# Performance work log

Measured on AMD Instinct MI355X. Metric: run time of the kernel, lower is better.

The kernel has to match this reference:

```python
import jax, jax.numpy as jnp
import numpy as np

N_NODES = 40000
N_EDGES = 640000
IN_DIM = 128
HID_DIM = 128


def _glorot(key, shape):
    fan_in, fan_out = shape[1], shape[0]
    lim = np.sqrt(6.0 / (fan_in + fan_out))
    return jax.random.uniform(key, shape, jnp.float32, -lim, lim)


def setup_inputs() -> dict:
    key = jax.random.key(0)
    ks = jax.random.split(key, 8)
    x = jax.random.normal(ks[0], (N_NODES, IN_DIM), dtype=jnp.float32)
    edge_index = jax.random.randint(ks[1], (2, N_EDGES), 0, N_NODES, dtype=jnp.int64)
    # SAGEConv params: lin_l (applied to aggregated neighbors, has bias), lin_r (self, no bias)
    W1l = _glorot(ks[2], (HID_DIM, IN_DIM))
    b1l = jnp.zeros((HID_DIM,), jnp.float32)
    W1r = _glorot(ks[3], (HID_DIM, IN_DIM))
    W2l = _glorot(ks[4], (HID_DIM, HID_DIM))
    b2l = jnp.zeros((HID_DIM,), jnp.float32)
    W2r = _glorot(ks[5], (HID_DIM, HID_DIM))
    return {"x": x, "edge_index": edge_index, "W1l": W1l, "b1l": b1l,
            "W1r": W1r, "W2l": W2l, "b2l": b2l, "W2r": W2r}


def _sage_conv(x, src, dst, Wl, bl, Wr):
    # mean aggregation of source features into destination nodes
    msg = x[src]  # [E, D] gather
    agg = jax.ops.segment_sum(msg, dst, num_segments=N_NODES)          # [N, D]
    cnt = jax.ops.segment_sum(jnp.ones_like(dst, jnp.float32), dst,
                              num_segments=N_NODES)                     # [N]
    mean = agg / jnp.maximum(cnt, 1.0)[:, None]
    # out = lin_l(mean_neighbors) + lin_r(x)
    return mean @ Wl.T + bl + x @ Wr.T


def reference(x, edge_index, W1l, b1l, W1r, W2l, b2l, W2r):
    src, dst = edge_index[0], edge_index[1]
    h = jax.nn.relu(_sage_conv(x, src, dst, W1l, b1l, W1r))
    h = jax.nn.relu(_sage_conv(h, src, dst, W2l, b2l, W2r))
    return h
```

## Files before the change

kernel.cpp:

```cpp
#include <hip/hip_runtime.h>
#include <hip/hip_bf16.h>

#define DIM 128
#define NN 40000
#define NE 640000
#define NBLK ((NN + 255) / 256)

typedef __attribute__((ext_vector_type(8))) short s16x8;
typedef __attribute__((ext_vector_type(4))) float f32x4;
typedef __attribute__((ext_vector_type(4))) unsigned short u16x4;
typedef __attribute__((ext_vector_type(4))) unsigned int u32x4;

__device__ __forceinline__ float bf16_lo(unsigned v) { return __uint_as_float(v << 16); }
__device__ __forceinline__ float bf16_hi(unsigned v) { return __uint_as_float(v & 0xffff0000u); }
__device__ __forceinline__ unsigned short f_to_bf16(float f) {
    unsigned u = __float_as_uint(f);
    u += 0x7fffu + ((u >> 16) & 1u);
    return (unsigned short)(u >> 16);
}

__global__ void fill_const_f32(float* __restrict__ out, int n, float v) {
    int i = blockIdx.x * blockDim.x + threadIdx.x;
    if (i < n) out[i] = v;
}

__global__ void cvt_all(const float* __restrict__ x, unsigned short* __restrict__ xb,
                        const float* __restrict__ w0, const float* __restrict__ w1,
                        const float* __restrict__ w2, const float* __restrict__ w3,
                        unsigned short* __restrict__ wb,
                        int* __restrict__ deg, const int* __restrict__ ei,
                        int* __restrict__ flag) {
    int b = blockIdx.x;
    if (b >= 5064) {
        int i = (b - 5064) * 256 + threadIdx.x;
        if (i < NN) deg[i] = 0;
        if (b == 5064 && threadIdx.x < 64) {
            int w = ei[2 * threadIdx.x + 1];
            unsigned long long m = __ballot(w == 0);
            if (threadIdx.x == 0) *flag = (m == ~0ull) ? 1 : 0;
        }
        return;
    }
    const float* src;
    unsigned short* dst;
    size_t i;
    if (b < 5000) {
        src = x; dst = xb;
        i = (size_t)b * 256 + threadIdx.x;
    } else {
        int w = b - 5000;
        int m = w >> 4;
        src = (m == 0) ? w0 : (m == 1) ? w1 : (m == 2) ? w2 : w3;
        dst = wb + (size_t)m * 16384;
        i = (size_t)(w & 15) * 256 + threadIdx.x;
    }
    f32x4 v = *(const f32x4*)(src + 4 * i);
    u16x4 o;
    o.x = f_to_bf16(v.x); o.y = f_to_bf16(v.y);
    o.z = f_to_bf16(v.z); o.w = f_to_bf16(v.w);
    *(u16x4*)(dst + 4 * i) = o;
}


__global__ void count_deg(const int* __restrict__ ei, const int* __restrict__ fmt,
                          int* __restrict__ deg) {
    int e = blockIdx.x * blockDim.x + threadIdx.x;
    if (e >= NE) return;
    int dst = (*fmt) ? ((const int2*)ei)[NE + e].x : ei[NE + e];
    if ((unsigned)dst < (unsigned)NN) atomicAdd(&deg[dst], 1);
}

__global__ void block_sums(const int* __restrict__ deg, int* __restrict__ bsum) {
    __shared__ int sh[256];
    int i = blockIdx.x * 256 + threadIdx.x;
    sh[threadIdx.x] = (i < NN) ? deg[i] : 0;
    __syncthreads();
    for (int off = 128; off > 0; off >>= 1) {
        if (threadIdx.x < off) sh[threadIdx.x] += sh[threadIdx.x + off];
        __syncthreads();
    }
    if (threadIdx.x == 0) bsum[blockIdx.x] = sh[0];
}

__global__ void scan_block2(const int* __restrict__ deg, const int* __restrict__ bsum,
                            int* __restrict__ row_ptr, int* __restrict__ cursor) {
    __shared__ int sh[256];
    int t = threadIdx.x, bid = blockIdx.x;

    int v0 = (t < NBLK) ? bsum[t] : 0;
    sh[t] = v0;
    __syncthreads();
    for (int off = 1; off < 256; off <<= 1) {
        int u = (t >= off) ? sh[t - off] : 0;
        __syncthreads();
        sh[t] += u;
        __syncthreads();
    }
    int base = sh[bid] - bsum[bid];
    __syncthreads();

    int i = bid * 256 + t;
    int v = (i < NN) ? deg[i] : 0;
    sh[t] = v;
    __syncthreads();
    for (int off = 1; off < 256; off <<= 1) {
        int u = (t >= off) ? sh[t - off] : 0;
        __syncthreads();
        sh[t] += u;
        __syncthreads();
    }
    int excl = sh[t] - v + base;
    if (i < NN) { row_ptr[i] = excl; cursor[i] = excl; }
    if (i == NN - 1) row_ptr[NN] = excl + v;
}

__global__ void fill_csr(const int* __restrict__ ei, const int* __restrict__ fmt,
                         int* __restrict__ cursor, int* __restrict__ sorted_src) {
    int e = blockIdx.x * blockDim.x + threadIdx.x;
    if (e >= NE) return;
    int src, dst;
    if (*fmt) {
        src = ((const int2*)ei)[e].x;
        dst = ((const int2*)ei)[NE + e].x;
    } else {
        src = ei[e];
        dst = ei[NE + e];
    }
    if ((unsigned)dst >= (unsigned)NN) return;
    int pos = atomicAdd(&cursor[dst], 1);
    if ((unsigned)pos < (unsigned)NE) sorted_src[pos] = src;
}


#define ACC8(A, v)                                 \
    A[0] += bf16_lo((v).x); A[1] += bf16_hi((v).x); \
    A[2] += bf16_lo((v).y); A[3] += bf16_hi((v).y); \
    A[4] += bf16_lo((v).z); A[5] += bf16_hi((v).z); \
    A[6] += bf16_lo((v).w); A[7] += bf16_hi((v).w);

__global__ __launch_bounds__(256) void aggregate_g(
    const unsigned short* __restrict__ xin,
    const int* __restrict__ row_ptr,
    const int* __restrict__ sorted_src,
    unsigned short* __restrict__ mean_out) {
    int lane = threadIdx.x & 63;
    int wv = threadIdx.x >> 6;
    int grp = lane >> 4;
    int lid = lane & 15;
    int gbase = grp << 4;
    int n = blockIdx.x * 16 + wv * 4 + grp;
    int start = row_ptr[n], end = row_ptr[n + 1];

    float a[8] = {0.f, 0.f, 0.f, 0.f, 0.f, 0.f, 0.f, 0.f};
    float b[8] = {0.f, 0.f, 0.f, 0.f, 0.f, 0.f, 0.f, 0.f};

    int i = start;
    for (; i + 16 <= end; i += 16) {
        int idx = sorted_src[i + lid];
#pragma unroll
        for (int j = 0; j < 16; j += 4) {
            int s0 = __shfl(idx, gbase + j);
            int s1 = __shfl(idx, gbase + j + 1);
            int s2 = __shfl(idx, gbase + j + 2);
            int s3 = __shfl(idx, gbase + j + 3);
            u32x4 v0 = *(const u32x4*)(xin + (size_t)s0 * DIM + lid * 8);
            u32x4 v1 = *(const u32x4*)(xin + (size_t)s1 * DIM + lid * 8);
            u32x4 v2 = *(const u32x4*)(xin + (size_t)s2 * DIM + lid * 8);
            u32x4 v3 = *(const u32x4*)(xin + (size_t)s3 * DIM + lid * 8);
            ACC8(a, v0);
            ACC8(b, v1);
            ACC8(a, v2);
            ACC8(b, v3);
        }
    }
    int rem = end - i;
    if (rem > 0) {
        int src_i = (i + lid < end) ? (i + lid) : (end - 1);
        int idx = sorted_src[src_i];
#pragma unroll
        for (int j = 0; j < 16; ++j) {
            if (j < rem) {
                int s = __shfl(idx, gbase + j);
                u32x4 v = *(const u32x4*)(xin + (size_t)s * DIM + lid * 8);
                if (j & 1) { ACC8(b, v); }
                else       { ACC8(a, v); }
            }
        }
    }

#pragma unroll
    for (int k = 0; k < 8; ++k) a[k] += b[k];

    int d = end - start;
    float inv = 1.f / (float)(d > 1 ? d : 1);
    u32x4 o;
    o.x = (unsigned)f_to_bf16(a[0] * inv) | ((unsigned)f_to_bf16(a[1] * inv) << 16);
    o.y = (unsigned)f_to_bf16(a[2] * inv) | ((unsigned)f_to_bf16(a[3] * inv) << 16);
    o.z = (unsigned)f_to_bf16(a[4] * inv) | ((unsigned)f_to_bf16(a[5] * inv) << 16);
    o.w = (unsigned)f_to_bf16(a[6] * inv) | ((unsigned)f_to_bf16(a[7] * inv) << 16);
    *(u32x4*)(mean_out + (size_t)n * DIM + lid * 8) = o;
}


template <bool WRITE_F32>
__global__ __launch_bounds__(256) void sage_gemm(
    const unsigned short* __restrict__ mean,
    const unsigned short* __restrict__ hself,
    const unsigned short* __restrict__ Wl,
    const unsigned short* __restrict__ Wr,
    const float* __restrict__ bias,
    void* __restrict__ outv) {
    int lane = threadIdx.x & 63;
    int wv = threadIdx.x >> 6;
    int quad = lane >> 4;
    int lid = lane & 15;
    int row0 = blockIdx.x * 64;
    int bcol = blockIdx.y * 64 + wv * 16 + lid;

    const unsigned short* wl0 = Wl + (size_t)bcol * DIM + quad * 8;
    const unsigned short* wr0 = Wr + (size_t)bcol * DIM + quad * 8;
    s16x8 bl[4], br[4];
#pragma unroll
    for (int kb = 0; kb < 4; ++kb) {
        bl[kb] = *(const s16x8*)(wl0 + kb * 32);
        br[kb] = *(const s16x8*)(wr0 + kb * 32);
    }

    const unsigned short* ap = mean + (size_t)(row0 + lid) * DIM + quad * 8;
    const unsigned short* hp = hself + (size_t)(row0 + lid) * DIM + quad * 8;
    const int TS = 16 * DIM;

    f32x4 acc[4] = {{0,0,0,0},{0,0,0,0},{0,0,0,0},{0,0,0,0}};
    s16x8 am[2][4], ah[2][4];

#pragma unroll
    for (int kb = 0; kb < 4; ++kb) {
        am[0][kb] = *(const s16x8*)(ap + kb * 32);
        ah[0][kb] = *(const s16x8*)(hp + kb * 32);
    }
#pragma unroll
    for (int t = 0; t < 4; ++t) {
        int cb = t & 1, nb = (t + 1) & 1;
        if (t < 3) {
#pragma unroll
            for (int kb = 0; kb < 4; ++kb) {
                am[nb][kb] = *(const s16x8*)(ap + (t + 1) * TS + kb * 32);
                ah[nb][kb] = *(const s16x8*)(hp + (t + 1) * TS + kb * 32);
            }
        }
#pragma unroll
        for (int kb = 0; kb < 4; ++kb)
            acc[t] = __builtin_amdgcn_mfma_f32_16x16x32_bf16(am[cb][kb], bl[kb], acc[t], 0, 0, 0);
#pragma unroll
        for (int kb = 0; kb < 4; ++kb)
            acc[t] = __builtin_amdgcn_mfma_f32_16x16x32_bf16(ah[cb][kb], br[kb], acc[t], 0, 0, 0);
    }

    float bv = bias[bcol];
#pragma unroll
    for (int t = 0; t < 4; ++t) {
#pragma unroll
        for (int r = 0; r < 4; ++r) {
            int orow = row0 + t * 16 + quad * 4 + r;
            float v = fmaxf(acc[t][r] + bv, 0.f);
            if (WRITE_F32)
                ((float*)outv)[(size_t)orow * DIM + bcol] = v;
            else
                ((unsigned short*)outv)[(size_t)orow * DIM + bcol] = f_to_bf16(v);
        }
    }
}


extern "C" void kernel_launch(void* const* d_in, const int* in_sizes, int n_in,
                              void* d_out, int out_size, void* d_ws, size_t ws_size,
                              hipStream_t stream) {
    const float* x   = (const float*)d_in[0];
    const int*   ei  = (const int*)d_in[1];
    const float* W1l = (const float*)d_in[2];
    const float* b1l = (const float*)d_in[3];
    const float* W1r = (const float*)d_in[4];
    const float* W2l = (const float*)d_in[5];
    const float* b2l = (const float*)d_in[6];
    const float* W2r = (const float*)d_in[7];
    float* out = (float*)d_out;

    const int OUT_ELEMS = NN * DIM;

    const size_t OFF_DEG  = 0;
    const size_t OFF_ROW  = 163840;
    const size_t OFF_BSUM = 324608;
    const size_t OFF_CUR  = 327680;
    const size_t OFF_FMT  = 491264;
    const size_t OFF_SRT  = 491520;
    const size_t OFF_WB   = 3051520;
    const size_t OFF_XB   = 3182592;
    const size_t OFF_MEAN = 13422592;
    const size_t OFF_H1   = 23662592;
    const size_t NEEDED   = 33902592;

    if (ws_size < NEEDED) {
        fill_const_f32<<<(OUT_ELEMS + 255) / 256, 256, 0, stream>>>(out, OUT_ELEMS, 50.0f);
        return;
    }

    char* ws = (char*)d_ws;
    int* deg     = (int*)(ws + OFF_DEG);
    int* row_ptr = (int*)(ws + OFF_ROW);
    int* bsum    = (int*)(ws + OFF_BSUM);
    int* cursor  = (int*)(ws + OFF_CUR);
    int* fmtflag = (int*)(ws + OFF_FMT);
    int* sorted  = (int*)(ws + OFF_SRT);
    unsigned short* Wb    = (unsigned short*)(ws + OFF_WB);
    unsigned short* xb    = (unsigned short*)(ws + OFF_XB);
    unsigned short* meanb = (unsigned short*)(ws + OFF_MEAN);
    unsigned short* h1b   = (unsigned short*)(ws + OFF_H1);
    unsigned short* W1lb = Wb;
    unsigned short* W1rb = Wb + 16384;
    unsigned short* W2lb = Wb + 32768;
    unsigned short* W2rb = Wb + 49152;

    cvt_all<<<5221, 256, 0, stream>>>(x, xb, W1l, W1r, W2l, W2r, Wb, deg, ei, fmtflag);
    count_deg<<<(NE + 255) / 256, 256, 0, stream>>>(ei, fmtflag, deg);
    block_sums<<<NBLK, 256, 0, stream>>>(deg, bsum);
    scan_block2<<<NBLK, 256, 0, stream>>>(deg, bsum, row_ptr, cursor);
    fill_csr<<<(NE + 255) / 256, 256, 0, stream>>>(ei, fmtflag, cursor, sorted);

    aggregate_g<<<NN / 16, 256, 0, stream>>>(xb, row_ptr, sorted, meanb);
    sage_gemm<false><<<dim3(NN / 64, 2), 256, 0, stream>>>(meanb, xb, W1lb, W1rb, b1l, h1b);

    aggregate_g<<<NN / 16, 256, 0, stream>>>(h1b, row_ptr, sorted, meanb);
    sage_gemm<true><<<dim3(NN / 64, 2), 256, 0, stream>>>(meanb, h1b, W2lb, W2rb, b2l, out);
}
```

Measured before the change: 248.7 us.

## Fuse neighbor aggregation and dual GEMM into one per-layer kernel via LDS

```diff
diff --git a/kernel.cpp b/kernel.cpp
--- a/kernel.cpp
+++ b/kernel.cpp
@@ -138,135 +138,140 @@
     A[4] += bf16_lo((v).z); A[5] += bf16_hi((v).z); \
     A[6] += bf16_lo((v).w); A[7] += bf16_hi((v).w);
 
-__global__ __launch_bounds__(256) void aggregate_g(
+template <bool WRITE_F32>
+__global__ __launch_bounds__(256) void sage_layer(
     const unsigned short* __restrict__ xin,
     const int* __restrict__ row_ptr,
     const int* __restrict__ sorted_src,
-    unsigned short* __restrict__ mean_out) {
-    int lane = threadIdx.x & 63;
-    int wv = threadIdx.x >> 6;
-    int grp = lane >> 4;
-    int lid = lane & 15;
-    int gbase = grp << 4;
-    int n = blockIdx.x * 16 + wv * 4 + grp;
-    int start = row_ptr[n], end = row_ptr[n + 1];
-
-    float a[8] = {0.f, 0.f, 0.f, 0.f, 0.f, 0.f, 0.f, 0.f};
-    float b[8] = {0.f, 0.f, 0.f, 0.f, 0.f, 0.f, 0.f, 0.f};
-
-    int i = start;
-    for (; i + 16 <= end; i += 16) {
-        int idx = sorted_src[i + lid];
-#pragma unroll
-        for (int j = 0; j < 16; j += 4) {
-            int s0 = __shfl(idx, gbase + j);
-            int s1 = __shfl(idx, gbase + j + 1);
-            int s2 = __shfl(idx, gbase + j + 2);
-            int s3 = __shfl(idx, gbase + j + 3);
-            u32x4 v0 = *(const u32x4*)(xin + (size_t)s0 * DIM + lid * 8);
-            u32x4 v1 = *(const u32x4*)(xin + (size_t)s1 * DIM + lid * 8);
-            u32x4 v2 = *(const u32x4*)(xin + (size_t)s2 * DIM + lid * 8);
-            u32x4 v3 = *(const u32x4*)(xin + (size_t)s3 * DIM + lid * 8);
-            ACC8(a, v0);
-            ACC8(b, v1);
-            ACC8(a, v2);
-            ACC8(b, v3);
-        }
-    }
-    int rem = end - i;
-    if (rem > 0) {
-        int src_i = (i + lid < end) ? (i + lid) : (end - 1);
-        int idx = sorted_src[src_i];
-#pragma unroll
-        for (int j = 0; j < 16; ++j) {
-            if (j < rem) {
-                int s = __shfl(idx, gbase + j);
-                u32x4 v = *(const u32x4*)(xin + (size_t)s * DIM + lid * 8);
-                if (j & 1) { ACC8(b, v); }
-                else       { ACC8(a, v); }
-            }
-        }
-    }
-
-#pragma unroll
-    for (int k = 0; k < 8; ++k) a[k] += b[k];
-
-    int d = end - start;
-    float inv = 1.f / (float)(d > 1 ? d : 1);
-    u32x4 o;
-    o.x = (unsigned)f_to_bf16(a[0] * inv) | ((unsigned)f_to_bf16(a[1] * inv) << 16);
-    o.y = (unsigned)f_to_bf16(a[2] * inv) | ((unsigned)f_to_bf16(a[3] * inv) << 16);
-    o.z = (unsigned)f_to_bf16(a[4] * inv) | ((unsigned)f_to_bf16(a[5] * inv) << 16);
-    o.w = (unsigned)f_to_bf16(a[6] * inv) | ((unsigned)f_to_bf16(a[7] * inv) << 16);
-    *(u32x4*)(mean_out + (size_t)n * DIM + lid * 8) = o;
-}
-
-
-template <bool WRITE_F32>
-__global__ __launch_bounds__(256) void sage_gemm(
-    const unsigned short* __restrict__ mean,
-    const unsigned short* __restrict__ hself,
     const unsigned short* __restrict__ Wl,
     const unsigned short* __restrict__ Wr,
     const float* __restrict__ bias,
     void* __restrict__ outv) {
-    int lane = threadIdx.x & 63;
-    int wv = threadIdx.x >> 6;
-    int quad = lane >> 4;
-    int lid = lane & 15;
+    __shared__ unsigned short lds_mean[64 * 128];
+    __shared__ unsigned short lds_hs[64 * 128];
+
+    int tid = threadIdx.x;
+    int lane = tid & 63;
+    int wv = tid >> 6;
     int row0 = blockIdx.x * 64;
-    int bcol = blockIdx.y * 64 + wv * 16 + lid;
-
-    const unsigned short* wl0 = Wl + (size_t)bcol * DIM + quad * 8;
-    const unsigned short* wr0 = Wr + (size_t)bcol * DIM + quad * 8;
-    s16x8 bl[4], br[4];
-#pragma unroll
-    for (int kb = 0; kb < 4; ++kb) {
-        bl[kb] = *(const s16x8*)(wl0 + kb * 32);
-        br[kb] = *(const s16x8*)(wr0 + kb * 32);
-    }
-
-    const unsigned short* ap = mean + (size_t)(row0 + lid) * DIM + quad * 8;
-    const unsigned short* hp = hself + (size_t)(row0 + lid) * DIM + quad * 8;
-    const int TS = 16 * DIM;
-
-    f32x4 acc[4] = {{0,0,0,0},{0,0,0,0},{0,0,0,0},{0,0,0,0}};
-    s16x8 am[2][4], ah[2][4];
-
-#pragma unroll
-    for (int kb = 0; kb < 4; ++kb) {
-        am[0][kb] = *(const s16x8*)(ap + kb * 32);
-        ah[0][kb] = *(const s16x8*)(hp + kb * 32);
-    }
-#pragma unroll
-    for (int t = 0; t < 4; ++t) {
-        int cb = t & 1, nb = (t + 1) & 1;
-        if (t < 3) {
+
+    {
+        int r = tid >> 2;
+        int c4 = tid & 3;
+        const unsigned short* src = xin + (size_t)(row0 + r) * DIM + c4 * 32;
+#pragma unroll
+        for (int c = 0; c < 4; ++c) {
+            int lid = c4 * 4 + c;
+            u32x4 v = *(const u32x4*)(src + c * 8);
+            int off = (r >> 4) * 2048 + (lid >> 2) * 512 + (lid & 3) * 128 + (r & 15) * 8;
+            *(u32x4*)(lds_hs + off) = v;
+        }
+    }
+
+    {
+        int grp = lane >> 4;
+        int lid = lane & 15;
+        int gbase = grp << 4;
+        for (int it = 0; it < 4; ++it) {
+            int nb = wv * 16 + it * 4 + grp;
+            int n = row0 + nb;
+            int start = row_ptr[n], end = row_ptr[n + 1];
+
+            float a[8] = {0.f, 0.f, 0.f, 0.f, 0.f, 0.f, 0.f, 0.f};
+            float b[8] = {0.f, 0.f, 0.f, 0.f, 0.f, 0.f, 0.f, 0.f};
+
+            int i = start;
+            for (; i + 16 <= end; i += 16) {
+                int idx = sorted_src[i + lid];
+#pragma unroll
+                for (int j = 0; j < 16; j += 4) {
+                    int s0 = __shfl(idx, gbase + j);
+                    int s1 = __shfl(idx, gbase + j + 1);
+                    int s2 = __shfl(idx, gbase + j + 2);
+                    int s3 = __shfl(idx, gbase + j + 3);
+                    u32x4 v0 = *(const u32x4*)(xin + (size_t)s0 * DIM + lid * 8);
+                    u32x4 v1 = *(const u32x4*)(xin + (size_t)s1 * DIM + lid * 8);
+                    u32x4 v2 = *(const u32x4*)(xin + (size_t)s2 * DIM + lid * 8);
+                    u32x4 v3 = *(const u32x4*)(xin + (size_t)s3 * DIM + lid * 8);
+                    ACC8(a, v0);
+                    ACC8(b, v1);
+                    ACC8(a, v2);
+                    ACC8(b, v3);
+                }
+            }
+            int rem = end - i;
+            if (rem > 0) {
+                int src_i = (i + lid < end) ? (i + lid) : (end - 1);
+                int idx = sorted_src[src_i];
+#pragma unroll
+                for (int j = 0; j < 16; ++j) {
+                    if (j < rem) {
+                        int s = __shfl(idx, gbase + j);
+                        u32x4 v = *(const u32x4*)(xin + (size_t)s * DIM + lid * 8);
+                        if (j & 1) { ACC8(b, v); }
+                        else       { ACC8(a, v); }
+                    }
+                }
+            }
+#pragma unroll
+            for (int k = 0; k < 8; ++k) a[k] += b[k];
+
+            int d = end - start;
+            float inv = 1.f / (float)(d > 1 ? d : 1);
+            u32x4 o;
+            o.x = (unsigned)f_to_bf16(a[0] * inv) | ((unsigned)f_to_bf16(a[1] * inv) << 16);
+            o.y = (unsigned)f_to_bf16(a[2] * inv) | ((unsigned)f_to_bf16(a[3] * inv) << 16);
+            o.z = (unsigned)f_to_bf16(a[4] * inv) | ((unsigned)f_to_bf16(a[5] * inv) << 16);
+            o.w = (unsigned)f_to_bf16(a[6] * inv) | ((unsigned)f_to_bf16(a[7] * inv) << 16);
+            int off = (nb >> 4) * 2048 + (lid >> 2) * 512 + (lid & 3) * 128 + (nb & 15) * 8;
+            *(u32x4*)(lds_mean + off) = o;
+        }
+    }
+
+    __syncthreads();
+
+    {
+        int quad = lane >> 4;
+        int m16 = lane & 15;
+        int lo = lane * 8;
+#pragma unroll
+        for (int ch = 0; ch < 2; ++ch) {
+            int bcol = ch * 64 + wv * 16 + m16;
+            const unsigned short* wl0 = Wl + (size_t)bcol * DIM + quad * 8;
+            const unsigned short* wr0 = Wr + (size_t)bcol * DIM + quad * 8;
+            s16x8 bl[4], br[4];
 #pragma unroll
             for (int kb = 0; kb < 4; ++kb) {
-                am[nb][kb] = *(const s16x8*)(ap + (t + 1) * TS + kb * 32);
-                ah[nb][kb] = *(const s16x8*)(hp + (t + 1) * TS + kb * 32);
-            }
-        }
-#pragma unroll
-        for (int kb = 0; kb < 4; ++kb)
-            acc[t] = __builtin_amdgcn_mfma_f32_16x16x32_bf16(am[cb][kb], bl[kb], acc[t], 0, 0, 0);
-#pragma unroll
-        for (int kb = 0; kb < 4; ++kb)
-            acc[t] = __builtin_amdgcn_mfma_f32_16x16x32_bf16(ah[cb][kb], br[kb], acc[t], 0, 0, 0);
-    }
-
-    float bv = bias[bcol];
-#pragma unroll
-    for (int t = 0; t < 4; ++t) {
-#pragma unroll
-        for (int r = 0; r < 4; ++r) {
-            int orow = row0 + t * 16 + quad * 4 + r;
-            float v = fmaxf(acc[t][r] + bv, 0.f);
-            if (WRITE_F32)
-                ((float*)outv)[(size_t)orow * DIM + bcol] = v;
-            else
-                ((unsigned short*)outv)[(size_t)orow * DIM + bcol] = f_to_bf16(v);
+                bl[kb] = *(const s16x8*)(wl0 + kb * 32);
+                br[kb] = *(const s16x8*)(wr0 + kb * 32);
+            }
+            f32x4 acc[4] = {{0,0,0,0},{0,0,0,0},{0,0,0,0},{0,0,0,0}};
+#pragma unroll
+            for (int t = 0; t < 4; ++t) {
+#pragma unroll
+                for (int kb = 0; kb < 4; ++kb) {
+                    s16x8 am = *(const s16x8*)(lds_mean + t * 2048 + kb * 512 + lo);
+                    acc[t] = __builtin_amdgcn_mfma_f32_16x16x32_bf16(am, bl[kb], acc[t], 0, 0, 0);
+                }
+#pragma unroll
+                for (int kb = 0; kb < 4; ++kb) {
+                    s16x8 ah = *(const s16x8*)(lds_hs + t * 2048 + kb * 512 + lo);
+                    acc[t] = __builtin_amdgcn_mfma_f32_16x16x32_bf16(ah, br[kb], acc[t], 0, 0, 0);
+                }
+            }
+            float bv = bias[bcol];
+#pragma unroll
+            for (int t = 0; t < 4; ++t) {
+#pragma unroll
+                for (int r = 0; r < 4; ++r) {
+                    int orow = row0 + t * 16 + quad * 4 + r;
+                    float v = fmaxf(acc[t][r] + bv, 0.f);
+                    if (WRITE_F32)
+                        ((float*)outv)[(size_t)orow * DIM + bcol] = v;
+                    else
+                        ((unsigned short*)outv)[(size_t)orow * DIM + bcol] = f_to_bf16(v);
+                }
+            }
         }
     }
 }
@@ -295,7 +300,6 @@
     const size_t OFF_SRT  = 491520;
     const size_t OFF_WB   = 3051520;
     const size_t OFF_XB   = 3182592;
-    const size_t OFF_MEAN = 13422592;
     const size_t OFF_H1   = 23662592;
     const size_t NEEDED   = 33902592;
 
@@ -313,7 +317,6 @@
     int* sorted  = (int*)(ws + OFF_SRT);
     unsigned short* Wb    = (unsigned short*)(ws + OFF_WB);
     unsigned short* xb    = (unsigned short*)(ws + OFF_XB);
-    unsigned short* meanb = (unsigned short*)(ws + OFF_MEAN);
     unsigned short* h1b   = (unsigned short*)(ws + OFF_H1);
     unsigned short* W1lb = Wb;
     unsigned short* W1rb = Wb + 16384;
@@ -326,9 +329,6 @@
     scan_block2<<<NBLK, 256, 0, stream>>>(deg, bsum, row_ptr, cursor);
     fill_csr<<<(NE + 255) / 256, 256, 0, stream>>>(ei, fmtflag, cursor, sorted);
 
-    aggregate_g<<<NN / 16, 256, 0, stream>>>(xb, row_ptr, sorted, meanb);
-    sage_gemm<false><<<dim3(NN / 64, 2), 256, 0, stream>>>(meanb, xb, W1lb, W1rb, b1l, h1b);
-
-    aggregate_g<<<NN / 16, 256, 0, stream>>>(h1b, row_ptr, sorted, meanb);
-    sage_gemm<true><<<dim3(NN / 64, 2), 256, 0, stream>>>(meanb, h1b, W2lb, W2rb, b2l, out);
-}
+    sage_layer<false><<<NN / 64, 256, 0, stream>>>(xb, row_ptr, sorted, W1lb, W1rb, b1l, h1b);
+    sage_layer<true><<<NN / 64, 256, 0, stream>>>(h1b, row_ptr, sorted, W2lb, W2rb, b2l, out);
+}
```

Result: faster. 233.8 us (-6.0%).
